# Kernel tuning notes

Measured on AMD Instinct MI355X. Metric: run time of the kernel, lower is better.

## Reference

```python
import jax, jax.numpy as jnp
import numpy as np

N = 100000   # nodes
E = 1600000  # edges
D = 128      # input_dim == hidden_dim
L = 3        # num_layers
G = 256      # graphs in batch
EPS = 1e-5   # BatchNorm eps


def setup_inputs() -> dict:
    key = jax.random.key(0)
    ks = jax.random.split(key, 10)
    x = jax.random.normal(ks[0], (N, D), dtype=jnp.float32)
    edge_index = jax.random.randint(ks[1], (2, E), 0, N, dtype=jnp.int64)
    batch = jnp.sort(jax.random.randint(ks[2], (N,), 0, G, dtype=jnp.int64))
    # stacked per-layer params (all layers are D->D since input_dim==hidden_dim)
    W = jax.random.normal(ks[3], (L, D, D), dtype=jnp.float32) * 0.05
    b = jax.random.normal(ks[4], (L, D), dtype=jnp.float32) * 0.02
    gamma = 1.0 + 0.1 * jax.random.normal(ks[5], (L, D), dtype=jnp.float32)
    beta = 0.1 * jax.random.normal(ks[6], (L, D), dtype=jnp.float32)
    rmean = 0.05 * jax.random.normal(ks[7], (L, D), dtype=jnp.float32)
    rvar = jax.random.uniform(ks[8], (L, D), minval=0.5, maxval=1.5, dtype=jnp.float32)
    return {"x": x, "W": W, "b": b, "gamma": gamma, "beta": beta,
            "rmean": rmean, "rvar": rvar, "edge_index": edge_index, "batch": batch}


def reference(x, W, b, gamma, beta, rmean, rvar, edge_index, batch):
    # --- GCN normalization with self-loops (same for every layer) ---
    src, dst = edge_index[0], edge_index[1]
    loop = jnp.arange(N, dtype=src.dtype)
    s = jnp.concatenate([src, loop])  # [E+N]
    d = jnp.concatenate([dst, loop])
    deg = jax.ops.segment_sum(jnp.ones(E + N, x.dtype), d, num_segments=N)
    dinv = jnp.where(deg > 0, jax.lax.rsqrt(deg), 0.0)
    norm = dinv[s] * dinv[d]  # [E+N]

    h = x
    for i in range(L):
        m = h @ W[i]                                            # [N, D] dense GEMM
        agg = jax.ops.segment_sum(m[s] * norm[:, None], d, num_segments=N)
        h = agg + b[i]
        # BatchNorm1d (inference: running stats), then ReLU; dropout is identity in eval
        h = (h - rmean[i]) * jax.lax.rsqrt(rvar[i] + EPS) * gamma[i] + beta[i]
        h = jax.nn.relu(h)

    # --- global mean / max pooling by graph id ---
    counts = jax.ops.segment_sum(jnp.ones(N, h.dtype), batch, num_segments=G)
    mean_pool = jax.ops.segment_sum(h, batch, num_segments=G) / jnp.maximum(counts, 1.0)[:, None]
    max_pool = jax.ops.segment_max(h, batch, num_segments=G)
    return jnp.concatenate([mean_pool, max_pool], axis=1)  # [G, 2D]
```

## Files before the change

### kernel.cpp

```cpp
#include <hip/hip_runtime.h>
#include <math.h>
#include <float.h>

#define D 128

typedef short short8 __attribute__((ext_vector_type(8)));
typedef float f32x4 __attribute__((ext_vector_type(4)));

__device__ __forceinline__ unsigned int bf16r(float f) {
    unsigned int u = __float_as_uint(f);
    return (u + 0x7fffu + ((u >> 16) & 1u)) >> 16;
}
__device__ __forceinline__ float bf2f(unsigned int lo16) {
    return __uint_as_float(lo16 << 16);
}

__global__ __launch_bounds__(256) void prep_fused(
    const int* __restrict__ dst, int* __restrict__ cnt, int* __restrict__ rank, int E,
    const float* __restrict__ W, const float* __restrict__ b,
    const float* __restrict__ gamma, const float* __restrict__ beta,
    const float* __restrict__ rmean, const float* __restrict__ rvar,
    unsigned short* __restrict__ Wt, float* __restrict__ sc, float* __restrict__ sh, int L_,
    const int* __restrict__ batch, int* __restrict__ gstart, int n, int G,
    int cb, int wb) {
    int blk = blockIdx.x;
    int tid = threadIdx.x;
    if (blk < cb) {
        int base = (blk * 256 + tid) * 4;
        if (base + 4 <= E) {
            int4 d = *(const int4*)&dst[base];
            int r0 = atomicAdd(&cnt[d.x], 1);
            int r1 = atomicAdd(&cnt[d.y], 1);
            int r2 = atomicAdd(&cnt[d.z], 1);
            int r3 = atomicAdd(&cnt[d.w], 1);
            *(int4*)&rank[base] = make_int4(r0, r1, r2, r3);
        } else if (base < E) {
            for (int e = base; e < E; ++e) rank[e] = atomicAdd(&cnt[dst[e]], 1);
        }
    } else if (blk < cb + wb) {
        int t = (blk - cb) * 256 + tid;
        int total = L_ * D * D;
        if (t < total) {
            int l = t / (D * D), rem = t % (D * D);
            int r = rem >> 7, k = rem & 127;
            Wt[t] = (unsigned short)bf16r(W[l * D * D + k * D + r]);
        }
        if (t < L_ * D) {
            float inv = rsqrtf(rvar[t] + 1e-5f);
            float s = inv * gamma[t];
            sc[t] = s;
            sh[t] = (b[t] - rmean[t]) * s + beta[t];
        }
    } else {
        int i = (blk - cb - wb) * 256 + tid;
        if (i >= n) return;
        int g = batch[i];
        int gp = (i == 0) ? -1 : batch[i - 1];
        for (int gg = gp + 1; gg <= g; ++gg) gstart[gg] = i;
        if (i == n - 1) for (int gg = g + 1; gg <= G; ++gg) gstart[gg] = n;
    }
}


__global__ void scan1(const int* __restrict__ cnt, int* __restrict__ rp, int* __restrict__ aux,
                      float* __restrict__ dinv, int n) {
    __shared__ int sh[256];
    int tid = threadIdx.x;
    int base = blockIdx.x * 1024 + tid * 4;
    int v[4]; int s = 0;
#pragma unroll
    for (int i = 0; i < 4; i++) {
        int idx = base + i;
        int t = (idx < n) ? cnt[idx] : 0;
        if (idx < n) dinv[idx] = rsqrtf((float)t + 1.0f);
        v[i] = s; s += t;
    }
    sh[tid] = s; __syncthreads();
    for (int off = 1; off < 256; off <<= 1) {
        int t = (tid >= off) ? sh[tid - off] : 0;
        __syncthreads();
        sh[tid] += t;
        __syncthreads();
    }
    int excl = sh[tid] - s;
#pragma unroll
    for (int i = 0; i < 4; i++) { int idx = base + i; if (idx < n) rp[idx] = excl + v[i]; }
    if (tid == 255) aux[blockIdx.x] = sh[255];
}

__global__ void scan2(int* aux, int nb) {
    __shared__ int sh[256];
    int tid = threadIdx.x;
    int v = (tid < nb) ? aux[tid] : 0;
    sh[tid] = v; __syncthreads();
    for (int off = 1; off < 256; off <<= 1) {
        int t = (tid >= off) ? sh[tid - off] : 0;
        __syncthreads();
        sh[tid] += t;
        __syncthreads();
    }
    if (tid < nb) aux[tid] = sh[tid] - v;
}

__global__ void scan3(int* __restrict__ rp, const int* __restrict__ aux, int n, int E) {
    int base = blockIdx.x * 1024;
    int add = aux[blockIdx.x];
    for (int i = threadIdx.x; i < 1024; i += 256) {
        int idx = base + i;
        if (idx < n) rp[idx] += add;
    }
    if (blockIdx.x == 0 && threadIdx.x == 0) rp[n] = E;
}

#define GBM 128
template<bool F32IN>
__device__ __forceinline__ void gemm_body_noA(short* Wl, const void* __restrict__ hin_v,
                                              const unsigned short* __restrict__ Wt,
                                              const float* __restrict__ dinv,
                                              unsigned short* __restrict__ mout, int n, int blk) {
    const int tid = threadIdx.x;
    const int row0 = blk * GBM;

#pragma unroll
    for (int i = 0; i < 4; ++i) {
        int c = tid + i * 512;
        int r = c >> 4, ck = (c & 15) * 8;
        *(int4*)&Wl[r * 136 + ck] = *(const int4*)&Wt[(size_t)r * D + ck];
    }
    __syncthreads();

    const int wid = tid >> 6;
    const int lane = tid & 63;
    const int lr = lane & 15;
    const int lg = lane >> 4;

    const int grow = row0 + wid * 16 + lr;
    const bool valid = grow < n;

    f32x4 acc[8];
#pragma unroll
    for (int fc = 0; fc < 8; ++fc) acc[fc] = (f32x4){0.f, 0.f, 0.f, 0.f};

#pragma unroll
    for (int ks = 0; ks < 4; ++ks) {
        int kb = ks * 32 + lg * 8;
        short8 y;
        if (F32IN) {
            const float* xf = (const float*)hin_v;
            float4 va = make_float4(0.f, 0.f, 0.f, 0.f);
            float4 vb = make_float4(0.f, 0.f, 0.f, 0.f);
            if (valid) {
                va = *(const float4*)&xf[(size_t)grow * D + kb];
                vb = *(const float4*)&xf[(size_t)grow * D + kb + 4];
            }
            uint4 pk;
            pk.x = bf16r(va.x) | (bf16r(va.y) << 16);
            pk.y = bf16r(va.z) | (bf16r(va.w) << 16);
            pk.z = bf16r(vb.x) | (bf16r(vb.y) << 16);
            pk.w = bf16r(vb.z) | (bf16r(vb.w) << 16);
            y = *(short8*)&pk;
        } else {
            const unsigned short* hb = (const unsigned short*)hin_v;
            if (valid) y = *(const short8*)&hb[(size_t)grow * D + kb];
            else { int4 z = make_int4(0, 0, 0, 0); y = *(short8*)&z; }
        }
#pragma unroll
        for (int fc = 0; fc < 8; ++fc) {
            short8 x = *(const short8*)&Wl[(fc * 16 + lr) * 136 + kb];
            acc[fc] = __builtin_amdgcn_mfma_f32_16x16x32_bf16(x, y, acc[fc], 0, 0, 0);
        }
    }

    if (valid) {
        float di = dinv[grow];
#pragma unroll
        for (int fc = 0; fc < 8; ++fc) {
            int gcol = fc * 16 + lg * 4;
            uint2 pk;
            pk.x = bf16r(acc[fc][0] * di) | (bf16r(acc[fc][1] * di) << 16);
            pk.y = bf16r(acc[fc][2] * di) | (bf16r(acc[fc][3] * di) << 16);
            *(uint2*)&mout[(size_t)grow * D + gcol] = pk;
        }
    }
}

__global__ __launch_bounds__(512) void fused_fill_gemm0(
    const float* __restrict__ x, const unsigned short* __restrict__ Wt,
    const float* __restrict__ dinv, unsigned short* __restrict__ mout, int n,
    const int* __restrict__ src, const int* __restrict__ dst,
    const int* __restrict__ rp, const int* __restrict__ rank,
    int* __restrict__ csr, int E, int gemmb) {
    __shared__ short Wl[D * 136];
    if ((int)blockIdx.x < gemmb) {
        gemm_body_noA<true>(Wl, (const void*)x, Wt, dinv, mout, n, blockIdx.x);
    } else {
        int gblk = blockIdx.x - gemmb;
        int base = (gblk * 512 + (int)threadIdx.x) * 4;
        if (base + 4 <= E) {
            int4 d = *(const int4*)&dst[base];
            int4 s = *(const int4*)&src[base];
            int4 r = *(const int4*)&rank[base];
            int p0 = rp[d.x];
            int p1 = rp[d.y];
            int p2 = rp[d.z];
            int p3 = rp[d.w];
            csr[p0 + r.x] = s.x;
            csr[p1 + r.y] = s.y;
            csr[p2 + r.z] = s.z;
            csr[p3 + r.w] = s.w;
        } else if (base < E) {
            for (int e = base; e < E; ++e) csr[rp[dst[e]] + rank[e]] = src[e];
        }
    }
}

template<bool F32IN>
__global__ __launch_bounds__(512) void gemm_mfma(const void* __restrict__ hin_v,
                                                 const unsigned short* __restrict__ Wt,
                                                 const float* __restrict__ dinv,
                                                 unsigned short* __restrict__ mout, int n) {
    __shared__ short Ah[GBM * 136];
    __shared__ short Wl[D * 136];
    const int tid = threadIdx.x;
    const int row0 = blockIdx.x * GBM;

#pragma unroll
    for (int i = 0; i < 4; ++i) {
        int c = tid + i * 512;
        int r = c >> 4, ck = (c & 15) * 8;
        int grow = row0 + r;
        if (F32IN) {
            const float* xf = (const float*)hin_v;
            float4 va = make_float4(0.f, 0.f, 0.f, 0.f);
            float4 vb = make_float4(0.f, 0.f, 0.f, 0.f);
            if (grow < n) {
                va = *(const float4*)&xf[(size_t)grow * D + ck];
                vb = *(const float4*)&xf[(size_t)grow * D + ck + 4];
            }
            uint4 pk;
            pk.x = bf16r(va.x) | (bf16r(va.y) << 16);
            pk.y = bf16r(va.z) | (bf16r(va.w) << 16);
            pk.z = bf16r(vb.x) | (bf16r(vb.y) << 16);
            pk.w = bf16r(vb.z) | (bf16r(vb.w) << 16);
            *(uint4*)&Ah[r * 136 + ck] = pk;
        } else {
            const unsigned short* hb = (const unsigned short*)hin_v;
            int4 v = make_int4(0, 0, 0, 0);
            if (grow < n) v = *(const int4*)&hb[(size_t)grow * D + ck];
            *(int4*)&Ah[r * 136 + ck] = v;
        }
    }
#pragma unroll
    for (int i = 0; i < 4; ++i) {
        int c = tid + i * 512;
        int r = c >> 4, ck = (c & 15) * 8;
        *(int4*)&Wl[r * 136 + ck] = *(const int4*)&Wt[(size_t)r * D + ck];
    }
    __syncthreads();

    const int wid = tid >> 6;
    const int lane = tid & 63;
    const int lr = lane & 15;
    const int lg = lane >> 4;

    f32x4 acc[8];
#pragma unroll
    for (int fc = 0; fc < 8; ++fc) acc[fc] = (f32x4){0.f, 0.f, 0.f, 0.f};

#pragma unroll
    for (int ks = 0; ks < 4; ++ks) {
        int kb = ks * 32 + lg * 8;
        short8 y = *(const short8*)&Ah[(wid * 16 + lr) * 136 + kb];
#pragma unroll
        for (int fc = 0; fc < 8; ++fc) {
            short8 x = *(const short8*)&Wl[(fc * 16 + lr) * 136 + kb];
            acc[fc] = __builtin_amdgcn_mfma_f32_16x16x32_bf16(x, y, acc[fc], 0, 0, 0);
        }
    }

    int grow = row0 + wid * 16 + lr;
    if (grow < n) {
        float di = dinv[grow];
#pragma unroll
        for (int fc = 0; fc < 8; ++fc) {
            int gcol = fc * 16 + lg * 4;
            uint2 pk;
            pk.x = bf16r(acc[fc][0] * di) | (bf16r(acc[fc][1] * di) << 16);
            pk.y = bf16r(acc[fc][2] * di) | (bf16r(acc[fc][3] * di) << 16);
            *(uint2*)&mout[(size_t)grow * D + gcol] = pk;
        }
    }
}

__global__ __launch_bounds__(256) void agg_bf16(const unsigned int* __restrict__ M,
                                                const int* __restrict__ rp,
                                                const int* __restrict__ csr,
                                                const float* __restrict__ dinv,
                                                const float* __restrict__ sc,
                                                const float* __restrict__ sh,
                                                unsigned int* __restrict__ H, int n) {
    const int wid = threadIdx.x >> 6;
    const int lane = threadIdx.x & 63;
    const int row = blockIdx.x * 4 + wid;
    if (row >= n) return;

    unsigned int u = M[(unsigned)row * 64u + lane];
    float a0 = bf2f(u & 0xffffu);
    float a1 = bf2f(u >> 16);

    int e = rp[row];
    const int end = rp[row + 1];
    const int n16 = (end - e) >> 4;

    if (n16 > 0) {
        int sa[16];
#pragma unroll
        for (int i = 0; i < 16; ++i) sa[i] = csr[e + i];
        for (int it = 0; it < n16; ++it) {
            int sb[16];
            if (it + 1 < n16) {
#pragma unroll
                for (int i = 0; i < 16; ++i) sb[i] = csr[e + 16 + i];
            } else {
#pragma unroll
                for (int i = 0; i < 16; ++i) sb[i] = 0;
            }
            unsigned int g[16];
#pragma unroll
            for (int i = 0; i < 16; ++i) g[i] = M[(unsigned)sa[i] * 64u + lane];
#pragma unroll
            for (int i = 0; i < 16; ++i) {
                a0 += bf2f(g[i] & 0xffffu);
                a1 += bf2f(g[i] >> 16);
            }
#pragma unroll
            for (int i = 0; i < 16; ++i) sa[i] = sb[i];
            e += 16;
        }
    }
    for (; e + 4 <= end; e += 4) {
        int s[4];
#pragma unroll
        for (int i = 0; i < 4; ++i) s[i] = csr[e + i];
        unsigned int g[4];
#pragma unroll
        for (int i = 0; i < 4; ++i) g[i] = M[(unsigned)s[i] * 64u + lane];
#pragma unroll
        for (int i = 0; i < 4; ++i) {
            a0 += bf2f(g[i] & 0xffffu);
            a1 += bf2f(g[i] >> 16);
        }
    }
    for (; e < end; ++e) {
        unsigned int gs = M[(unsigned)csr[e] * 64u + lane];
        a0 += bf2f(gs & 0xffffu);
        a1 += bf2f(gs >> 16);
    }

    float di = dinv[row];
    int c0 = lane * 2;
    float v0 = fmaxf(a0 * di * sc[c0] + sh[c0], 0.f);
    float v1 = fmaxf(a1 * di * sc[c0 + 1] + sh[c0 + 1], 0.f);
    H[(unsigned)row * 64u + lane] = bf16r(v0) | (bf16r(v1) << 16);
}

__global__ __launch_bounds__(64) void pool1(const unsigned int* __restrict__ H,
                                            const int* __restrict__ gstart,
                                            float4* __restrict__ pbuf) {
    int g = blockIdx.x, c = blockIdx.y;
    int lane = threadIdx.x;
    int beg = gstart[g], end = gstart[g + 1];
    int len = end - beg;
    int cb = beg + (int)(((long long)len * c) >> 3);
    int ce = beg + (int)(((long long)len * (c + 1)) >> 3);
    float s0 = 0.f, s1 = 0.f, m0 = -INFINITY, m1 = -INFINITY;
    int i = cb;
    for (; i + 2 <= ce; i += 2) {
        unsigned int ua = H[(size_t)i * 64 + lane];
        unsigned int ub = H[(size_t)(i + 1) * 64 + lane];
        float a0 = bf2f(ua & 0xffffu), a1 = bf2f(ua >> 16);
        float b0 = bf2f(ub & 0xffffu), b1 = bf2f(ub >> 16);
        s0 += a0 + b0; s1 += a1 + b1;
        m0 = fmaxf(m0, fmaxf(a0, b0)); m1 = fmaxf(m1, fmaxf(a1, b1));
    }
    for (; i < ce; ++i) {
        unsigned int ua = H[(size_t)i * 64 + lane];
        float a0 = bf2f(ua & 0xffffu), a1 = bf2f(ua >> 16);
        s0 += a0; s1 += a1;
        m0 = fmaxf(m0, a0); m1 = fmaxf(m1, a1);
    }
    pbuf[((size_t)g * 8 + c) * 64 + lane] = make_float4(s0, s1, m0, m1);
}

__global__ __launch_bounds__(64) void pool2(const float4* __restrict__ pbuf,
                                            const int* __restrict__ gstart,
                                            float* __restrict__ out) {
    int g = blockIdx.x;
    int lane = threadIdx.x;
    float s0 = 0.f, s1 = 0.f, m0 = -INFINITY, m1 = -INFINITY;
#pragma unroll
    for (int c = 0; c < 8; ++c) {
        float4 p = pbuf[((size_t)g * 8 + c) * 64 + lane];
        s0 += p.x; s1 += p.y;
        m0 = fmaxf(m0, p.z); m1 = fmaxf(m1, p.w);
    }
    float cnt = fmaxf((float)(gstart[g + 1] - gstart[g]), 1.0f);
    int c0 = lane * 2;
    out[g * (2 * D) + c0] = s0 / cnt;
    out[g * (2 * D) + c0 + 1] = s1 / cnt;
    out[g * (2 * D) + D + c0] = m0;
    out[g * (2 * D) + D + c0 + 1] = m1;
}

extern "C" void kernel_launch(void* const* d_in, const int* in_sizes, int n_in,
                              void* d_out, int out_size, void* d_ws, size_t ws_size,
                              hipStream_t stream) {
    const float* x     = (const float*)d_in[0];
    const float* W     = (const float*)d_in[1];
    const float* b     = (const float*)d_in[2];
    const float* gamma = (const float*)d_in[3];
    const float* beta  = (const float*)d_in[4];
    const float* rmean = (const float*)d_in[5];
    const float* rvar  = (const float*)d_in[6];
    const int*   eidx  = (const int*)d_in[7];
    const int*   batch = (const int*)d_in[8];

    const int N = in_sizes[8];
    const int E = in_sizes[7] / 2;
    const int L = in_sizes[2] / D;
    const int G = out_size / (2 * D);

    const int* esrc = eidx;
    const int* edst = eidx + E;

    size_t off = 0;
    auto carve = [&](size_t bytes) { size_t cur = off; off += (bytes + 255) & ~(size_t)255; return cur; };
    char* base = (char*)d_ws;
    const int nb = (N + 1023) / 1024;

    int*            cnt  = (int*)           (base + carve((size_t)N * 4));
    int*            rp   = (int*)           (base + carve((size_t)(N + 1) * 4));
    int*            aux  = (int*)           (base + carve((size_t)nb * 4));
    float*          dinv = (float*)         (base + carve((size_t)N * 4));
    int*            rank = (int*)           (base + carve((size_t)E * 4));
    int*            csr  = (int*)           (base + carve((size_t)E * 4));
    unsigned short* hbuf = (unsigned short*)(base + carve((size_t)N * D * 2));
    unsigned short* mbuf = (unsigned short*)(base + carve((size_t)N * D * 2));
    unsigned short* Wt   = (unsigned short*)(base + carve((size_t)L * D * D * 2));
    float*          sc   = (float*)         (base + carve((size_t)L * D * 4));
    float*          shb  = (float*)         (base + carve((size_t)L * D * 4));
    int*            gst  = (int*)           (base + carve((size_t)(G + 1) * 4));
    float4*         pbuf = (float4*)        (base + carve((size_t)G * 8 * 64 * 16));
    (void)ws_size;

    hipMemsetAsync(cnt, 0, (size_t)N * 4, stream);

    const int cb = ((E + 3) / 4 + 255) / 256;
    const int wb = (L * D * D + 255) / 256;
    const int bb = (N + 255) / 256;
    const int gemmb = (N + GBM - 1) / GBM;
    const int fb = ((E + 3) / 4 + 511) / 512;
    const int aggb = (N + 3) / 4;

    prep_fused<<<cb + wb + bb, 256, 0, stream>>>(edst, cnt, rank, E,
                                                 W, b, gamma, beta, rmean, rvar,
                                                 Wt, sc, shb, L,
                                                 batch, gst, N, G, cb, wb);
    scan1<<<nb, 256, 0, stream>>>(cnt, rp, aux, dinv, N);
    scan2<<<1, 256, 0, stream>>>(aux, nb);
    scan3<<<nb, 256, 0, stream>>>(rp, aux, N, E);

    fused_fill_gemm0<<<gemmb + fb, 512, 0, stream>>>(x, Wt, dinv, mbuf, N,
                                                     esrc, edst, rp, rank, csr, E, gemmb);
    agg_bf16<<<aggb, 256, 0, stream>>>((const unsigned int*)mbuf, rp, csr, dinv,
                                       sc, shb, (unsigned int*)hbuf, N);

    for (int l = 1; l < L; ++l) {
        gemm_mfma<false><<<gemmb, 512, 0, stream>>>((const void*)hbuf, Wt + (size_t)l * D * D,
                                                    dinv, mbuf, N);
        agg_bf16<<<aggb, 256, 0, stream>>>((const unsigned int*)mbuf, rp, csr, dinv,
                                           sc + l * D, shb + l * D,
                                           (unsigned int*)hbuf, N);
    }

    pool1<<<dim3(G, 8), 64, 0, stream>>>((const unsigned int*)hbuf, gst, pbuf);
    pool2<<<G, 64, 0, stream>>>(pbuf, gst, (float*)d_out);
}
```

Measured before the change: 367.9 us.

## Move layer-0 GEMM into prep kernel and fold scan3 into consumers

The first-layer GEMM moves into the prep kernel, where it runs alongside the degree-counting atomics. It uses weights converted from fp32 on the fly and writes unscaled bf16 results. The dinv row scaling becomes a separate pass fused with the CSR fill kernel. The scan3 kernel is removed: the fill and aggregation kernels add the per-block scan offset themselves, so one launch is saved. The cost is an extra read and write of the message buffer for scaling, a second bf16 rounding step, and an extra aux lookup on every edge and row.

```diff
diff --git a/kernel.cpp b/kernel.cpp
--- a/kernel.cpp
+++ b/kernel.cpp
@@ -15,16 +15,19 @@
     return __uint_as_float(lo16 << 16);
 }
 
+#define GBM0 64
 __global__ __launch_bounds__(256) void prep_fused(
     const int* __restrict__ dst, int* __restrict__ cnt, int* __restrict__ rank, int E,
+    const float* __restrict__ x, unsigned short* __restrict__ mraw, int n,
     const float* __restrict__ W, const float* __restrict__ b,
     const float* __restrict__ gamma, const float* __restrict__ beta,
     const float* __restrict__ rmean, const float* __restrict__ rvar,
     unsigned short* __restrict__ Wt, float* __restrict__ sc, float* __restrict__ sh, int L_,
-    const int* __restrict__ batch, int* __restrict__ gstart, int n, int G,
-    int cb, int wb) {
-    int blk = blockIdx.x;
-    int tid = threadIdx.x;
+    const int* __restrict__ batch, int* __restrict__ gstart, int G,
+    int cb, int gb, int wb) {
+    __shared__ short Wl[D * 136];
+    const int blk = blockIdx.x;
+    const int tid = threadIdx.x;
     if (blk < cb) {
         int base = (blk * 256 + tid) * 4;
         if (base + 4 <= E) {
@@ -37,8 +40,61 @@
         } else if (base < E) {
             for (int e = base; e < E; ++e) rank[e] = atomicAdd(&cnt[dst[e]], 1);
         }
-    } else if (blk < cb + wb) {
-        int t = (blk - cb) * 256 + tid;
+    } else if (blk < cb + gb) {
+#pragma unroll
+        for (int i = 0; i < 64; ++i) {
+            int t = i * 256 + tid;
+            int k = t >> 7, r = t & 127;
+            Wl[r * 136 + k] = (short)bf16r(W[t]);
+        }
+        __syncthreads();
+
+        const int row0 = (blk - cb) * GBM0;
+        const int wid = tid >> 6;
+        const int lane = tid & 63;
+        const int lr = lane & 15;
+        const int lg = lane >> 4;
+        const int grow = row0 + wid * 16 + lr;
+        const bool valid = grow < n;
+
+        f32x4 acc[8];
+#pragma unroll
+        for (int fc = 0; fc < 8; ++fc) acc[fc] = (f32x4){0.f, 0.f, 0.f, 0.f};
+
+#pragma unroll
+        for (int ks = 0; ks < 4; ++ks) {
+            int kb = ks * 32 + lg * 8;
+            float4 va = make_float4(0.f, 0.f, 0.f, 0.f);
+            float4 vb = make_float4(0.f, 0.f, 0.f, 0.f);
+            if (valid) {
+                va = *(const float4*)&x[(size_t)grow * D + kb];
+                vb = *(const float4*)&x[(size_t)grow * D + kb + 4];
+            }
+            uint4 pk;
+            pk.x = bf16r(va.x) | (bf16r(va.y) << 16);
+            pk.y = bf16r(va.z) | (bf16r(va.w) << 16);
+            pk.z = bf16r(vb.x) | (bf16r(vb.y) << 16);
+            pk.w = bf16r(vb.z) | (bf16r(vb.w) << 16);
+            short8 y = *(short8*)&pk;
+#pragma unroll
+            for (int fc = 0; fc < 8; ++fc) {
+                short8 xf = *(const short8*)&Wl[(fc * 16 + lr) * 136 + kb];
+                acc[fc] = __builtin_amdgcn_mfma_f32_16x16x32_bf16(xf, y, acc[fc], 0, 0, 0);
+            }
+        }
+
+        if (valid) {
+#pragma unroll
+            for (int fc = 0; fc < 8; ++fc) {
+                int gcol = fc * 16 + lg * 4;
+                uint2 pk;
+                pk.x = bf16r(acc[fc][0]) | (bf16r(acc[fc][1]) << 16);
+                pk.y = bf16r(acc[fc][2]) | (bf16r(acc[fc][3]) << 16);
+                *(uint2*)&mraw[(size_t)grow * D + gcol] = pk;
+            }
+        }
+    } else if (blk < cb + gb + wb) {
+        int t = (blk - cb - gb) * 256 + tid;
         int total = L_ * D * D;
         if (t < total) {
             int l = t / (D * D), rem = t % (D * D);
@@ -52,7 +108,7 @@
             sh[t] = (b[t] - rmean[t]) * s + beta[t];
         }
     } else {
-        int i = (blk - cb - wb) * 256 + tid;
+        int i = (blk - cb - gb - wb) * 256 + tid;
         if (i >= n) return;
         int g = batch[i];
         int gp = (i == 0) ? -1 : batch[i - 1];
@@ -102,120 +158,50 @@
     if (tid < nb) aux[tid] = sh[tid] - v;
 }
 
-__global__ void scan3(int* __restrict__ rp, const int* __restrict__ aux, int n, int E) {
-    int base = blockIdx.x * 1024;
-    int add = aux[blockIdx.x];
-    for (int i = threadIdx.x; i < 1024; i += 256) {
-        int idx = base + i;
-        if (idx < n) rp[idx] += add;
-    }
-    if (blockIdx.x == 0 && threadIdx.x == 0) rp[n] = E;
-}
-
-#define GBM 128
-template<bool F32IN>
-__device__ __forceinline__ void gemm_body_noA(short* Wl, const void* __restrict__ hin_v,
-                                              const unsigned short* __restrict__ Wt,
-                                              const float* __restrict__ dinv,
-                                              unsigned short* __restrict__ mout, int n, int blk) {
+__global__ __launch_bounds__(256) void fill_scale(
+    const int* __restrict__ src, const int* __restrict__ dst,
+    const int* __restrict__ rp, const int* __restrict__ aux,
+    const int* __restrict__ rank, int* __restrict__ csr, int E,
+    unsigned int* __restrict__ M, const float* __restrict__ dinv, int n,
+    int fb) {
+    const int blk = blockIdx.x;
     const int tid = threadIdx.x;
-    const int row0 = blk * GBM;
-
-#pragma unroll
-    for (int i = 0; i < 4; ++i) {
-        int c = tid + i * 512;
-        int r = c >> 4, ck = (c & 15) * 8;
-        *(int4*)&Wl[r * 136 + ck] = *(const int4*)&Wt[(size_t)r * D + ck];
-    }
-    __syncthreads();
-
-    const int wid = tid >> 6;
-    const int lane = tid & 63;
-    const int lr = lane & 15;
-    const int lg = lane >> 4;
-
-    const int grow = row0 + wid * 16 + lr;
-    const bool valid = grow < n;
-
-    f32x4 acc[8];
-#pragma unroll
-    for (int fc = 0; fc < 8; ++fc) acc[fc] = (f32x4){0.f, 0.f, 0.f, 0.f};
-
-#pragma unroll
-    for (int ks = 0; ks < 4; ++ks) {
-        int kb = ks * 32 + lg * 8;
-        short8 y;
-        if (F32IN) {
-            const float* xf = (const float*)hin_v;
-            float4 va = make_float4(0.f, 0.f, 0.f, 0.f);
-            float4 vb = make_float4(0.f, 0.f, 0.f, 0.f);
-            if (valid) {
-                va = *(const float4*)&xf[(size_t)grow * D + kb];
-                vb = *(const float4*)&xf[(size_t)grow * D + kb + 4];
-            }
-            uint4 pk;
-            pk.x = bf16r(va.x) | (bf16r(va.y) << 16);
-            pk.y = bf16r(va.z) | (bf16r(va.w) << 16);
-            pk.z = bf16r(vb.x) | (bf16r(vb.y) << 16);
-            pk.w = bf16r(vb.z) | (bf16r(vb.w) << 16);
-            y = *(short8*)&pk;
-        } else {
-            const unsigned short* hb = (const unsigned short*)hin_v;
-            if (valid) y = *(const short8*)&hb[(size_t)grow * D + kb];
-            else { int4 z = make_int4(0, 0, 0, 0); y = *(short8*)&z; }
-        }
-#pragma unroll
-        for (int fc = 0; fc < 8; ++fc) {
-            short8 x = *(const short8*)&Wl[(fc * 16 + lr) * 136 + kb];
-            acc[fc] = __builtin_amdgcn_mfma_f32_16x16x32_bf16(x, y, acc[fc], 0, 0, 0);
-        }
-    }
-
-    if (valid) {
-        float di = dinv[grow];
-#pragma unroll
-        for (int fc = 0; fc < 8; ++fc) {
-            int gcol = fc * 16 + lg * 4;
-            uint2 pk;
-            pk.x = bf16r(acc[fc][0] * di) | (bf16r(acc[fc][1] * di) << 16);
-            pk.y = bf16r(acc[fc][2] * di) | (bf16r(acc[fc][3] * di) << 16);
-            *(uint2*)&mout[(size_t)grow * D + gcol] = pk;
-        }
-    }
-}
-
-__global__ __launch_bounds__(512) void fused_fill_gemm0(
-    const float* __restrict__ x, const unsigned short* __restrict__ Wt,
-    const float* __restrict__ dinv, unsigned short* __restrict__ mout, int n,
-    const int* __restrict__ src, const int* __restrict__ dst,
-    const int* __restrict__ rp, const int* __restrict__ rank,
-    int* __restrict__ csr, int E, int gemmb) {
-    __shared__ short Wl[D * 136];
-    if ((int)blockIdx.x < gemmb) {
-        gemm_body_noA<true>(Wl, (const void*)x, Wt, dinv, mout, n, blockIdx.x);
-    } else {
-        int gblk = blockIdx.x - gemmb;
-        int base = (gblk * 512 + (int)threadIdx.x) * 4;
+    if (blk < fb) {
+        int base = (blk * 256 + tid) * 4;
         if (base + 4 <= E) {
             int4 d = *(const int4*)&dst[base];
             int4 s = *(const int4*)&src[base];
             int4 r = *(const int4*)&rank[base];
-            int p0 = rp[d.x];
-            int p1 = rp[d.y];
-            int p2 = rp[d.z];
-            int p3 = rp[d.w];
+            int p0 = rp[d.x] + aux[d.x >> 10];
+            int p1 = rp[d.y] + aux[d.y >> 10];
+            int p2 = rp[d.z] + aux[d.z >> 10];
+            int p3 = rp[d.w] + aux[d.w >> 10];
             csr[p0 + r.x] = s.x;
             csr[p1 + r.y] = s.y;
             csr[p2 + r.z] = s.z;
             csr[p3 + r.w] = s.w;
         } else if (base < E) {
-            for (int e = base; e < E; ++e) csr[rp[dst[e]] + rank[e]] = src[e];
-        }
-    }
-}
-
-template<bool F32IN>
-__global__ __launch_bounds__(512) void gemm_mfma(const void* __restrict__ hin_v,
+            for (int e = base; e < E; ++e)
+                csr[rp[dst[e]] + aux[dst[e] >> 10] + rank[e]] = src[e];
+        }
+    } else {
+        int t = (blk - fb) * 256 + tid;
+        int total4 = n * 16;
+        if (t >= total4) return;
+        int row = t >> 4;
+        float di = dinv[row];
+        uint4 v = *(uint4*)&M[(size_t)t * 4];
+        uint4 o;
+        o.x = bf16r(bf2f(v.x & 0xffffu) * di) | (bf16r(bf2f(v.x >> 16) * di) << 16);
+        o.y = bf16r(bf2f(v.y & 0xffffu) * di) | (bf16r(bf2f(v.y >> 16) * di) << 16);
+        o.z = bf16r(bf2f(v.z & 0xffffu) * di) | (bf16r(bf2f(v.z >> 16) * di) << 16);
+        o.w = bf16r(bf2f(v.w & 0xffffu) * di) | (bf16r(bf2f(v.w >> 16) * di) << 16);
+        *(uint4*)&M[(size_t)t * 4] = o;
+    }
+}
+
+#define GBM 128
+__global__ __launch_bounds__(512) void gemm_mfma(const unsigned short* __restrict__ hin,
                                                  const unsigned short* __restrict__ Wt,
                                                  const float* __restrict__ dinv,
                                                  unsigned short* __restrict__ mout, int n) {
@@ -229,26 +215,9 @@
         int c = tid + i * 512;
         int r = c >> 4, ck = (c & 15) * 8;
         int grow = row0 + r;
-        if (F32IN) {
-            const float* xf = (const float*)hin_v;
-            float4 va = make_float4(0.f, 0.f, 0.f, 0.f);
-            float4 vb = make_float4(0.f, 0.f, 0.f, 0.f);
-            if (grow < n) {
-                va = *(const float4*)&xf[(size_t)grow * D + ck];
-                vb = *(const float4*)&xf[(size_t)grow * D + ck + 4];
-            }
-            uint4 pk;
-            pk.x = bf16r(va.x) | (bf16r(va.y) << 16);
-            pk.y = bf16r(va.z) | (bf16r(va.w) << 16);
-            pk.z = bf16r(vb.x) | (bf16r(vb.y) << 16);
-            pk.w = bf16r(vb.z) | (bf16r(vb.w) << 16);
-            *(uint4*)&Ah[r * 136 + ck] = pk;
-        } else {
-            const unsigned short* hb = (const unsigned short*)hin_v;
-            int4 v = make_int4(0, 0, 0, 0);
-            if (grow < n) v = *(const int4*)&hb[(size_t)grow * D + ck];
-            *(int4*)&Ah[r * 136 + ck] = v;
-        }
+        int4 v = make_int4(0, 0, 0, 0);
+        if (grow < n) v = *(const int4*)&hin[(size_t)grow * D + ck];
+        *(int4*)&Ah[r * 136 + ck] = v;
     }
 #pragma unroll
     for (int i = 0; i < 4; ++i) {
@@ -273,8 +242,8 @@
         short8 y = *(const short8*)&Ah[(wid * 16 + lr) * 136 + kb];
 #pragma unroll
         for (int fc = 0; fc < 8; ++fc) {
-            short8 x = *(const short8*)&Wl[(fc * 16 + lr) * 136 + kb];
-            acc[fc] = __builtin_amdgcn_mfma_f32_16x16x32_bf16(x, y, acc[fc], 0, 0, 0);
+            short8 xf = *(const short8*)&Wl[(fc * 16 + lr) * 136 + kb];
+            acc[fc] = __builtin_amdgcn_mfma_f32_16x16x32_bf16(xf, y, acc[fc], 0, 0, 0);
         }
     }
 
@@ -294,11 +263,12 @@
 
 __global__ __launch_bounds__(256) void agg_bf16(const unsigned int* __restrict__ M,
                                                 const int* __restrict__ rp,
+                                                const int* __restrict__ aux,
                                                 const int* __restrict__ csr,
                                                 const float* __restrict__ dinv,
                                                 const float* __restrict__ sc,
                                                 const float* __restrict__ sh,
-                                                unsigned int* __restrict__ H, int n) {
+                                                unsigned int* __restrict__ H, int n, int Etot) {
     const int wid = threadIdx.x >> 6;
     const int lane = threadIdx.x & 63;
     const int row = blockIdx.x * 4 + wid;
@@ -308,8 +278,8 @@
     float a0 = bf2f(u & 0xffffu);
     float a1 = bf2f(u >> 16);
 
-    int e = rp[row];
-    const int end = rp[row + 1];
+    int e = rp[row] + aux[row >> 10];
+    const int end = (row + 1 < n) ? rp[row + 1] + aux[(row + 1) >> 10] : Etot;
     const int n16 = (end - e) >> 4;
 
     if (n16 > 0) {
@@ -456,31 +426,33 @@
     hipMemsetAsync(cnt, 0, (size_t)N * 4, stream);
 
     const int cb = ((E + 3) / 4 + 255) / 256;
+    const int gb = (N + GBM0 - 1) / GBM0;
     const int wb = (L * D * D + 255) / 256;
     const int bb = (N + 255) / 256;
     const int gemmb = (N + GBM - 1) / GBM;
-    const int fb = ((E + 3) / 4 + 511) / 512;
+    const int fb = ((E + 3) / 4 + 255) / 256;
+    const int sb = (N * 16 + 255) / 256;
     const int aggb = (N + 3) / 4;
 
-    prep_fused<<<cb + wb + bb, 256, 0, stream>>>(edst, cnt, rank, E,
-                                                 W, b, gamma, beta, rmean, rvar,
-                                                 Wt, sc, shb, L,
-                                                 batch, gst, N, G, cb, wb);
+    prep_fused<<<cb + gb + wb + bb, 256, 0, stream>>>(edst, cnt, rank, E,
+                                                      x, mbuf, N,
+                                                      W, b, gamma, beta, rmean, rvar,
+                                                      Wt, sc, shb, L,
+                                                      batch, gst, G, cb, gb, wb);
     scan1<<<nb, 256, 0, stream>>>(cnt, rp, aux, dinv, N);
     scan2<<<1, 256, 0, stream>>>(aux, nb);
-    scan3<<<nb, 256, 0, stream>>>(rp, aux, N, E);
-
-    fused_fill_gemm0<<<gemmb + fb, 512, 0, stream>>>(x, Wt, dinv, mbuf, N,
-                                                     esrc, edst, rp, rank, csr, E, gemmb);
-    agg_bf16<<<aggb, 256, 0, stream>>>((const unsigned int*)mbuf, rp, csr, dinv,
-                                       sc, shb, (unsigned int*)hbuf, N);
+
+    fill_scale<<<fb + sb, 256, 0, stream>>>(esrc, edst, rp, aux, rank, csr, E,
+                                            (unsigned int*)mbuf, dinv, N, fb);
+
+    agg_bf16<<<aggb, 256, 0, stream>>>((const unsigned int*)mbuf, rp, aux, csr, dinv,
+                                       sc, shb, (unsigned int*)hbuf, N, E);
 
     for (int l = 1; l < L; ++l) {
-        gemm_mfma<false><<<gemmb, 512, 0, stream>>>((const void*)hbuf, Wt + (size_t)l * D * D,
-                                                    dinv, mbuf, N);
-        agg_bf16<<<aggb, 256, 0, stream>>>((const unsigned int*)mbuf, rp, csr, dinv,
+        gemm_mfma<<<gemmb, 512, 0, stream>>>(hbuf, Wt + (size_t)l * D * D, dinv, mbuf, N);
+        agg_bf16<<<aggb, 256, 0, stream>>>((const unsigned int*)mbuf, rp, aux, csr, dinv,
                                            sc + l * D, shb + l * D,
-                                           (unsigned int*)hbuf, N);
+                                           (unsigned int*)hbuf, N, E);
     }
 
     pool1<<<dim3(G, 8), 64, 0, stream>>>((const unsigned int*)hbuf, gst, pbuf);
```

Result: slower. 375.6 us (+2.1%).
